# Kernel tuning notes

Measured on AMD Instinct MI355X. Metric: run time of the kernel, lower is better.

Reference implementation:

```python
import jax, jax.numpy as jnp
import numpy as np

N = 50000   # nodes
E = 200000  # edges (avg degree ~4, pose-graph-like sparsity)
F_IN = 512
NEG_SLOPE = 0.01  # F.leaky_relu default


def _softmax_aggr(src_feat, dst, num_nodes):
    # torch_geometric SoftmaxAggregation(t=1): per-destination, per-feature
    # alpha = softmax(x_j), out = sum_j alpha * x_j
    m = jax.ops.segment_max(src_feat, dst, num_segments=num_nodes)  # [N,F]
    m = jnp.where(jnp.isfinite(m), m, 0.0)  # empty segments -> -inf guard
    e = jnp.exp(src_feat - m[dst])                                   # [E,F]
    denom = jax.ops.segment_sum(e, dst, num_segments=num_nodes)      # [N,F]
    num = jax.ops.segment_sum(e * src_feat, dst, num_segments=num_nodes)
    return num / jnp.maximum(denom, 1e-16)  # 0 for isolated nodes


def setup_inputs() -> dict:
    key = jax.random.key(0)
    ks = jax.random.split(key, 9)
    inp = {
        "x": jax.random.normal(ks[0], (N, F_IN), dtype=jnp.float32),
        "W1_rel": jax.random.normal(ks[1], (513, 256), dtype=jnp.float32) * 0.04,
        "b1_rel": jnp.zeros((256,), dtype=jnp.float32),
        "W1_root": jax.random.normal(ks[2], (513, 256), dtype=jnp.float32) * 0.04,
        "W2_rel": jax.random.normal(ks[3], (257, 64), dtype=jnp.float32) * 0.06,
        "b2_rel": jnp.zeros((64,), dtype=jnp.float32),
        "W2_root": jax.random.normal(ks[4], (257, 64), dtype=jnp.float32) * 0.06,
        "Wp": jax.random.normal(ks[5], (65, 3), dtype=jnp.float32) * 0.1,
        "bp": jnp.zeros((3,), dtype=jnp.float32),
        "Wr": jax.random.normal(ks[6], (65, 4), dtype=jnp.float32) * 0.1,
        "br": jnp.zeros((4,), dtype=jnp.float32),
        "edge_index": jax.random.randint(ks[7], (2, E), 0, N, dtype=jnp.int64),
    }
    return inp


def reference(x, W1_rel, b1_rel, W1_root, W2_rel, b2_rel, W2_root,
              Wp, bp, Wr, br, edge_index):
    src, dst = edge_index[0], edge_index[1]
    node_index = jnp.arange(x.shape[0], dtype=x.dtype)[:, None]  # [N,1]

    # dropout is identity in eval mode
    h = jnp.concatenate([x, node_index], axis=1)  # [N,513]

    # GraphConv(513,256, aggr='softmax'): lin_rel(softmax_aggr(x_j)) + lin_root(x)
    agg1 = _softmax_aggr(h[src], dst, x.shape[0])               # [N,513]
    h = agg1 @ W1_rel + b1_rel + h @ W1_root                     # [N,256]
    h = jnp.where(h >= 0, h, NEG_SLOPE * h)

    h = jnp.concatenate([h, node_index], axis=1)  # [N,257]

    # GraphConv(257,64) default aggr='add'
    agg2 = jax.ops.segment_sum(h[src], dst, num_segments=x.shape[0])  # [N,257]
    h = agg2 @ W2_rel + b2_rel + h @ W2_root                           # [N,64]
    h = jnp.where(h >= 0, h, NEG_SLOPE * h)

    h = jnp.concatenate([h, node_index], axis=1)  # [N,65]

    position = h @ Wp + bp                         # [N,3]
    rotation = h @ Wr + br                         # [N,4]
    norm = jnp.linalg.norm(rotation, axis=1, keepdims=True)
    rotation = rotation / jnp.maximum(norm, 1e-12)  # F.normalize

    return jnp.concatenate([position, rotation], axis=1)  # [N,7]
```

## Files before the change

### kernel.cpp

```cpp
#include <hip/hip_runtime.h>

#define NNODES 50000
#define NEDGES 200000
#define NSCANB ((NNODES + 255) / 256)

typedef short  bf16x8 __attribute__((ext_vector_type(8)));
typedef float  f32x4  __attribute__((ext_vector_type(4)));
typedef unsigned int u32x4 __attribute__((ext_vector_type(4)));

__device__ __forceinline__ unsigned short f2bf(float f) {
    union { float f; unsigned int u; } c; c.f = f;
    unsigned int r = c.u + 0x7fffu + ((c.u >> 16) & 1u);
    return (unsigned short)(r >> 16);
}
__device__ __forceinline__ float bf2f(unsigned short h) {
    union { unsigned int u; float f; } c; c.u = ((unsigned int)h) << 16;
    return c.f;
}
__device__ __forceinline__ float bflo(unsigned int v) {
    union { unsigned int u; float f; } c; c.u = v << 16;
    return c.f;
}
__device__ __forceinline__ float bfhi(unsigned int v) {
    union { unsigned int u; float f; } c; c.u = v & 0xffff0000u;
    return c.f;
}

#define PREP_B1 (256 * 1024)
#define PREP_B2 (64 * 512)
#define PREP_XC (NNODES * 64)
__global__ __launch_bounds__(256) void k_prepcount(const float* __restrict__ x,
                                                   const float* __restrict__ W1_rel,
                                                   const float* __restrict__ W1_root,
                                                   const float* __restrict__ W2_rel,
                                                   const float* __restrict__ W2_root,
                                                   const int* __restrict__ ei,
                                                   int* __restrict__ deg,
                                                   unsigned short* __restrict__ Bt1,
                                                   unsigned short* __restrict__ Bt2,
                                                   unsigned short* __restrict__ xb) {
    const int gtid = blockIdx.x * 256 + threadIdx.x;
    const int GS = gridDim.x * 256;
    for (int e = gtid; e < NEDGES; e += GS) atomicAdd(&deg[ei[NEDGES + e]], 1);
    for (int i = gtid; i < PREP_B1; i += GS) {
        int n = i >> 10, k = i & 1023;
        float v = (k < 512) ? W1_rel[k * 256 + n] : W1_root[(k - 512) * 256 + n];
        Bt1[i] = f2bf(v);
    }
    for (int i = gtid; i < PREP_B2; i += GS) {
        int n = i >> 9, k = i & 511;
        float v = (k < 256) ? W2_rel[k * 64 + n] : W2_root[(k - 256) * 64 + n];
        Bt2[i] = f2bf(v);
    }
    for (int i = gtid; i < PREP_XC; i += GS) {
        int n = i >> 6, c8 = (i & 63) * 8;
        const float* xp = x + (size_t)n * 512 + c8;
        float4 a = *(const float4*)xp;
        float4 bb = *(const float4*)(xp + 4);
        unsigned short o[8];
        o[0] = f2bf(a.x); o[1] = f2bf(a.y); o[2] = f2bf(a.z); o[3] = f2bf(a.w);
        o[4] = f2bf(bb.x); o[5] = f2bf(bb.y); o[6] = f2bf(bb.z); o[7] = f2bf(bb.w);
        *(u32x4*)(xb + (size_t)n * 512 + c8) = *(const u32x4*)o;
    }
}

__global__ __launch_bounds__(256) void k_scanA(const int* __restrict__ deg,
                                               int* __restrict__ rs,
                                               int* __restrict__ partials) {
    __shared__ int sm[256];
    int t = threadIdx.x, i = blockIdx.x * 256 + t;
    int v = (i < NNODES) ? deg[i] : 0;
    sm[t] = v;
    __syncthreads();
#pragma unroll
    for (int off = 1; off < 256; off <<= 1) {
        int u = (t >= off) ? sm[t - off] : 0;
        __syncthreads();
        sm[t] += u;
        __syncthreads();
    }
    if (i < NNODES) rs[i] = sm[t] - v;
    if (t == 255) partials[blockIdx.x] = sm[255];
}

__global__ __launch_bounds__(256) void k_scanC2(int* __restrict__ rs,
                                                const int* __restrict__ partials,
                                                int* __restrict__ cursor) {
    __shared__ int sm[256];
    int t = threadIdx.x, b = blockIdx.x;
    sm[t] = (t < b && t < NSCANB) ? partials[t] : 0;
    __syncthreads();
#pragma unroll
    for (int off = 128; off; off >>= 1) {
        if (t < off) sm[t] += sm[t + off];
        __syncthreads();
    }
    int off0 = sm[0];
    int i = b * 256 + t;
    if (i < NNODES) {
        int rv = rs[i] + off0;
        rs[i] = rv;
        cursor[i] = rv;
    }
    if (i == 0) rs[NNODES] = NEDGES;
}

__global__ void k_scatter(const int* __restrict__ ei, int* __restrict__ cursor,
                          int* __restrict__ srcs) {
    int e = blockIdx.x * 256 + threadIdx.x;
    if (e < NEDGES) {
        int d = ei[NEDGES + e];
        int p = atomicAdd(&cursor[d], 1);
        srcs[p] = ei[e];
    }
}

__global__ __launch_bounds__(256) void k_agg1(const unsigned short* __restrict__ xb,
                                              const int* __restrict__ rs,
                                              const int* __restrict__ srcs,
                                              unsigned short* __restrict__ AggBuf) {
    int wv = threadIdx.x >> 6;
    int lane = threadIdx.x & 63;
    int n = blockIdx.x * 4 + wv;
    int e0 = rs[n], e1 = rs[n + 1];
    float nu[8], de[8];
#pragma unroll
    for (int j = 0; j < 8; ++j) { nu[j] = 0.f; de[j] = 0.f; }
    int e = e0;
    for (; e + 1 < e1; e += 2) {
        int s0 = srcs[e], s1 = srcs[e + 1];
        u32x4 r0 = *(const u32x4*)(xb + (size_t)s0 * 512 + lane * 8);
        u32x4 r1 = *(const u32x4*)(xb + (size_t)s1 * 512 + lane * 8);
#pragma unroll
        for (int p = 0; p < 4; ++p) {
            float v0 = bflo(r0[p]), v1 = bfhi(r0[p]);
            float E0 = __expf(v0), E1 = __expf(v1);
            de[2 * p] += E0; nu[2 * p] += E0 * v0;
            de[2 * p + 1] += E1; nu[2 * p + 1] += E1 * v1;
        }
#pragma unroll
        for (int p = 0; p < 4; ++p) {
            float v0 = bflo(r1[p]), v1 = bfhi(r1[p]);
            float E0 = __expf(v0), E1 = __expf(v1);
            de[2 * p] += E0; nu[2 * p] += E0 * v0;
            de[2 * p + 1] += E1; nu[2 * p + 1] += E1 * v1;
        }
    }
    if (e < e1) {
        int s0 = srcs[e];
        u32x4 r0 = *(const u32x4*)(xb + (size_t)s0 * 512 + lane * 8);
#pragma unroll
        for (int p = 0; p < 4; ++p) {
            float v0 = bflo(r0[p]), v1 = bfhi(r0[p]);
            float E0 = __expf(v0), E1 = __expf(v1);
            de[2 * p] += E0; nu[2 * p] += E0 * v0;
            de[2 * p + 1] += E1; nu[2 * p + 1] += E1 * v1;
        }
    }
    unsigned short o[8];
#pragma unroll
    for (int j = 0; j < 8; ++j) o[j] = f2bf(nu[j] / fmaxf(de[j], 1e-16f));
    *(u32x4*)(AggBuf + (size_t)n * 512 + lane * 8) = *(const u32x4*)o;
}

__global__ __launch_bounds__(256) void k_agg2(const int* __restrict__ rs,
                                              const int* __restrict__ srcs,
                                              const unsigned short* __restrict__ H1,
                                              unsigned short* __restrict__ Seg) {
    int wv = threadIdx.x >> 6;
    int lane = threadIdx.x & 63;
    int n = blockIdx.x * 4 + wv;
    int e0 = rs[n], e1 = rs[n + 1];
    float a[4] = {0.f, 0.f, 0.f, 0.f};
    int e = e0;
    for (; e + 1 < e1; e += 2) {
        int s0 = srcs[e], s1 = srcs[e + 1];
        uint2 r0 = *(const uint2*)(H1 + (size_t)s0 * 256 + lane * 4);
        uint2 r1 = *(const uint2*)(H1 + (size_t)s1 * 256 + lane * 4);
        a[0] += bflo(r0.x) + bflo(r1.x);
        a[1] += bfhi(r0.x) + bfhi(r1.x);
        a[2] += bflo(r0.y) + bflo(r1.y);
        a[3] += bfhi(r0.y) + bfhi(r1.y);
    }
    if (e < e1) {
        uint2 r0 = *(const uint2*)(H1 + (size_t)srcs[e] * 256 + lane * 4);
        a[0] += bflo(r0.x); a[1] += bfhi(r0.x);
        a[2] += bflo(r0.y); a[3] += bfhi(r0.y);
    }
    uint2 o;
    o.x = (unsigned int)f2bf(a[0]) | ((unsigned int)f2bf(a[1]) << 16);
    o.y = (unsigned int)f2bf(a[2]) | ((unsigned int)f2bf(a[3]) << 16);
    *(uint2*)(Seg + (size_t)n * 256 + lane * 4) = o;
}

__global__ __launch_bounds__(256, 5) void k_gemm1(const unsigned short* __restrict__ A1,
                                                  const unsigned short* __restrict__ A2,
                                                  const unsigned short* __restrict__ Bt,
                                                  const int* __restrict__ rs,
                                                  const int* __restrict__ srcs,
                                                  const float* __restrict__ r1,
                                                  const float* __restrict__ r2,
                                                  const float* __restrict__ bias,
                                                  unsigned short* __restrict__ outp) {
    constexpr int BM = 64, BN = 128, BK = 64;
    __shared__ __align__(16) unsigned short As[2][BM * BK];
    __shared__ __align__(16) unsigned short Bs[2][BN * BK];
    __shared__ float s1t[BM];

    const int tid = threadIdx.x;
    const int w = tid >> 6;
    const int lane = tid & 63;
    const int lm = lane & 15;
    const int quad = lane >> 4;
    const int wr = w >> 1;
    const int wc = w & 1;
    const int rowbase = blockIdx.y * BM;
    const int colbase = blockIdx.x * BN;
    const int wrow = wr * 32;
    const int wcol = wc * 64;

    const int rsub = lane >> 3;
    const int csw = (lane & 7) ^ rsub;

    f32x4 acc[2][4];
#pragma unroll
    for (int mi = 0; mi < 2; ++mi)
#pragma unroll
        for (int ni = 0; ni < 4; ++ni) acc[mi][ni] = (f32x4){0.f, 0.f, 0.f, 0.f};

    auto stage = [&](unsigned short* Asb, unsigned short* Bsb, int kt) {
        const unsigned short* Ab = (kt < 512) ? A1 : A2;
        int kof = (kt < 512) ? kt : kt - 512;
#pragma unroll
        for (int l = 0; l < 2; ++l) {
            int r = w * 16 + l * 8;
            int gr = rowbase + r + rsub;
            if (gr >= NNODES) gr = NNODES - 1;
            const unsigned short* gp = Ab + (size_t)gr * 512 + kof + csw * 8;
            __builtin_amdgcn_global_load_lds(
                (const __attribute__((address_space(1))) void*)gp,
                (__attribute__((address_space(3))) void*)(Asb + r * BK), 16, 0, 0);
        }
#pragma unroll
        for (int l = 0; l < 4; ++l) {
            int r = w * 32 + l * 8;
            const unsigned short* gp = Bt + (size_t)(colbase + r + rsub) * 1024 + kt + csw * 8;
            __builtin_amdgcn_global_load_lds(
                (const __attribute__((address_space(1))) void*)gp,
                (__attribute__((address_space(3))) void*)(Bsb + r * BK), 16, 0, 0);
        }
    };

    auto compute = [&](const unsigned short* Asb, const unsigned short* Bsb) {
#pragma unroll
        for (int kk = 0; kk < BK; kk += 32) {
            const int kidx = (kk >> 3) + quad;
            const int phys = kidx ^ (lm & 7);
            bf16x8 af[2], bfr[4];
#pragma unroll
            for (int mi = 0; mi < 2; ++mi)
                af[mi] = __builtin_bit_cast(bf16x8,
                    *(const u32x4*)(Asb + (wrow + mi * 16 + lm) * BK + phys * 8));
#pragma unroll
            for (int ni = 0; ni < 4; ++ni)
                bfr[ni] = __builtin_bit_cast(bf16x8,
                    *(const u32x4*)(Bsb + (wcol + ni * 16 + lm) * BK + phys * 8));
#pragma unroll
            for (int mi = 0; mi < 2; ++mi)
#pragma unroll
                for (int ni = 0; ni < 4; ++ni)
                    acc[mi][ni] = __builtin_amdgcn_mfma_f32_16x16x32_bf16(
                        af[mi], bfr[ni], acc[mi][ni], 0, 0, 0);
        }
    };

    stage(As[0], Bs[0], 0);
#pragma unroll 1
    for (int t = 0; t < 16; t += 2) {
        stage(As[1], Bs[1], (t + 1) * BK);
        asm volatile("s_waitcnt vmcnt(6)" ::: "memory");
        __builtin_amdgcn_s_barrier();
        __builtin_amdgcn_sched_barrier(0);
        compute(As[0], Bs[0]);
        __builtin_amdgcn_s_barrier();
        if (t + 2 < 16) {
            stage(As[0], Bs[0], (t + 2) * BK);
            asm volatile("s_waitcnt vmcnt(6)" ::: "memory");
        } else {
            asm volatile("s_waitcnt vmcnt(0)" ::: "memory");
        }
        __builtin_amdgcn_s_barrier();
        __builtin_amdgcn_sched_barrier(0);
        compute(As[1], Bs[1]);
        __builtin_amdgcn_s_barrier();
    }

    if (tid < BM) {
        int grow = rowbase + tid;
        float r_ = 0.f;
        if (grow < NNODES) {
            int e0 = rs[grow], e1 = rs[grow + 1];
            float m = -INFINITY, d = 0.f, q = 0.f;
            for (int e = e0; e < e1; ++e) {
                float v = (float)srcs[e];
                float nm = fmaxf(m, v);
                float sc = __expf(m - nm), ee = __expf(v - nm);
                d = d * sc + ee;
                q = q * sc + ee * v;
                m = nm;
            }
            r_ = q / fmaxf(d, 1e-16f);
        }
        s1t[tid] = r_;
    }
    __syncthreads();

#pragma unroll
    for (int ni = 0; ni < 4; ++ni) {
        int gc = colbase + wcol + ni * 16 + lm;
        float r1v = r1[gc], r2v = r2[gc], bv = bias[gc];
#pragma unroll
        for (int mi = 0; mi < 2; ++mi) {
#pragma unroll
            for (int r = 0; r < 4; ++r) {
                int lrow = wrow + mi * 16 + quad * 4 + r;
                int grow = rowbase + lrow;
                if (grow < NNODES) {
                    float v = acc[mi][ni][r] + s1t[lrow] * r1v + (float)grow * r2v + bv;
                    v = (v >= 0.f) ? v : 0.01f * v;
                    outp[(size_t)grow * 256 + gc] = f2bf(v);
                }
            }
        }
    }
}

__global__ __launch_bounds__(256) void k_gemm2h(const unsigned short* __restrict__ A1,
                                                const unsigned short* __restrict__ A2,
                                                const unsigned short* __restrict__ Bt,
                                                const int* __restrict__ rs,
                                                const int* __restrict__ srcs,
                                                const float* __restrict__ r1,
                                                const float* __restrict__ r2,
                                                const float* __restrict__ bias,
                                                const float* __restrict__ Wp,
                                                const float* __restrict__ bp,
                                                const float* __restrict__ Wr,
                                                const float* __restrict__ br,
                                                float* __restrict__ out) {
    constexpr int BM = 64, BN = 64, BK = 64;
    __shared__ __align__(16) unsigned short As[2][BM * BK];
    __shared__ __align__(16) unsigned short Bs[2][BN * BK];
    __shared__ float h2t[BM * 65];
    __shared__ float s1t[BM];

    const int tid = threadIdx.x;
    const int w = tid >> 6;
    const int lane = tid & 63;
    const int lm = lane & 15;
    const int quad = lane >> 4;
    const int rowbase = blockIdx.x * BM;
    const int wrow = w * 16;

    const int rsub = lane >> 3;
    const int csw = (lane & 7) ^ rsub;

    f32x4 acc[4];
#pragma unroll
    for (int ni = 0; ni < 4; ++ni) acc[ni] = (f32x4){0.f, 0.f, 0.f, 0.f};

    auto stage = [&](unsigned short* Asb, unsigned short* Bsb, int kt) {
        const unsigned short* Ab = (kt < 256) ? A1 : A2;
        int kof = (kt < 256) ? kt : kt - 256;
#pragma unroll
        for (int l = 0; l < 2; ++l) {
            int r = w * 16 + l * 8;
            int gr = rowbase + r + rsub;
            if (gr >= NNODES) gr = NNODES - 1;
            const unsigned short* gp = Ab + (size_t)gr * 256 + kof + csw * 8;
            __builtin_amdgcn_global_load_lds(
                (const __attribute__((address_space(1))) void*)gp,
                (__attribute__((address_space(3))) void*)(Asb + r * BK), 16, 0, 0);
        }
#pragma unroll
        for (int l = 0; l < 2; ++l) {
            int r = w * 16 + l * 8;
            const unsigned short* gp = Bt + (size_t)(r + rsub) * 512 + kt + csw * 8;
            __builtin_amdgcn_global_load_lds(
                (const __attribute__((address_space(1))) void*)gp,
                (__attribute__((address_space(3))) void*)(Bsb + r * BK), 16, 0, 0);
        }
    };

    auto compute = [&](const unsigned short* Asb, const unsigned short* Bsb) {
#pragma unroll
        for (int kk = 0; kk < BK; kk += 32) {
            const int kidx = (kk >> 3) + quad;
            const int phys = kidx ^ (lm & 7);
            bf16x8 af;
            af = __builtin_bit_cast(bf16x8,
                *(const u32x4*)(Asb + (wrow + lm) * BK + phys * 8));
            bf16x8 bfr[4];
#pragma unroll
            for (int ni = 0; ni < 4; ++ni)
                bfr[ni] = __builtin_bit_cast(bf16x8,
                    *(const u32x4*)(Bsb + (ni * 16 + lm) * BK + phys * 8));
#pragma unroll
            for (int ni = 0; ni < 4; ++ni)
                acc[ni] = __builtin_amdgcn_mfma_f32_16x16x32_bf16(
                    af, bfr[ni], acc[ni], 0, 0, 0);
        }
    };

    stage(As[0], Bs[0], 0);
#pragma unroll 1
    for (int t = 0; t < 8; t += 2) {
        stage(As[1], Bs[1], (t + 1) * BK);
        asm volatile("s_waitcnt vmcnt(4)" ::: "memory");
        __builtin_amdgcn_s_barrier();
        __builtin_amdgcn_sched_barrier(0);
        compute(As[0], Bs[0]);
        __builtin_amdgcn_s_barrier();
        if (t + 2 < 8) {
            stage(As[0], Bs[0], (t + 2) * BK);
            asm volatile("s_waitcnt vmcnt(4)" ::: "memory");
        } else {
            asm volatile("s_waitcnt vmcnt(0)" ::: "memory");
        }
        __builtin_amdgcn_s_barrier();
        __builtin_amdgcn_sched_barrier(0);
        compute(As[1], Bs[1]);
        __builtin_amdgcn_s_barrier();
    }

    if (tid < BM) {
        int grow = rowbase + tid;
        float si = 0.f;
        if (grow < NNODES) {
            int e0 = rs[grow], e1 = rs[grow + 1];
            for (int e = e0; e < e1; ++e) si += (float)srcs[e];
        }
        s1t[tid] = si;
    }
    __syncthreads();

#pragma unroll
    for (int ni = 0; ni < 4; ++ni) {
        int gc = ni * 16 + lm;
        float r1v = r1[gc], r2v = r2[gc], bv = bias[gc];
#pragma unroll
        for (int r = 0; r < 4; ++r) {
            int lrow = wrow + quad * 4 + r;
            int grow = rowbase + lrow;
            float v = acc[ni][r] + s1t[lrow] * r1v + (float)grow * r2v + bv;
            v = (v >= 0.f) ? v : 0.01f * v;
            h2t[lrow * 65 + gc] = v;
        }
    }
    __syncthreads();

    if (tid < BM) {
        int grow = rowbase + tid;
        if (grow < NNODES) {
            const float* hv = h2t + tid * 65;
            float idx = (float)grow;
            float p0 = 0.f, p1 = 0.f, p2 = 0.f;
            float r0 = 0.f, r1a = 0.f, r2a = 0.f, r3 = 0.f;
#pragma unroll 8
            for (int c = 0; c < 64; ++c) {
                float v = hv[c];
                p0 += v * Wp[c * 3 + 0];
                p1 += v * Wp[c * 3 + 1];
                p2 += v * Wp[c * 3 + 2];
                r0 += v * Wr[c * 4 + 0];
                r1a += v * Wr[c * 4 + 1];
                r2a += v * Wr[c * 4 + 2];
                r3 += v * Wr[c * 4 + 3];
            }
            p0 += idx * Wp[64 * 3 + 0] + bp[0];
            p1 += idx * Wp[64 * 3 + 1] + bp[1];
            p2 += idx * Wp[64 * 3 + 2] + bp[2];
            r0 += idx * Wr[64 * 4 + 0] + br[0];
            r1a += idx * Wr[64 * 4 + 1] + br[1];
            r2a += idx * Wr[64 * 4 + 2] + br[2];
            r3 += idx * Wr[64 * 4 + 3] + br[3];
            float nrm = fmaxf(sqrtf(r0 * r0 + r1a * r1a + r2a * r2a + r3 * r3), 1e-12f);
            float* op = out + (size_t)grow * 7;
            op[0] = p0; op[1] = p1; op[2] = p2;
            op[3] = r0 / nrm; op[4] = r1a / nrm; op[5] = r2a / nrm; op[6] = r3 / nrm;
        }
    }
}

extern "C" void kernel_launch(void* const* d_in, const int* in_sizes, int n_in,
                              void* d_out, int out_size, void* d_ws, size_t ws_size,
                              hipStream_t stream) {
    const float* x       = (const float*)d_in[0];
    const float* W1_rel  = (const float*)d_in[1];
    const float* b1      = (const float*)d_in[2];
    const float* W1_root = (const float*)d_in[3];
    const float* W2_rel  = (const float*)d_in[4];
    const float* b2      = (const float*)d_in[5];
    const float* W2_root = (const float*)d_in[6];
    const float* Wp      = (const float*)d_in[7];
    const float* bp      = (const float*)d_in[8];
    const float* Wr      = (const float*)d_in[9];
    const float* br      = (const float*)d_in[10];
    const int*   ei      = (const int*)d_in[11];
    float* out = (float*)d_out;

    char* ws = (char*)d_ws;
    size_t off = 0;
    auto alloc = [&](size_t bytes) {
        size_t o = off;
        off = (off + bytes + 255) & ~(size_t)255;
        return (void*)(ws + o);
    };
    int*   deg       = (int*)alloc(NNODES * 4);
    int*   cursor    = (int*)alloc(NNODES * 4);
    int*   row_start = (int*)alloc((NNODES + 1) * 4);
    int*   srcs      = (int*)alloc(NEDGES * 4);
    int*   partials  = (int*)alloc(NSCANB * 4);
    unsigned short* xb     = (unsigned short*)alloc((size_t)NNODES * 512 * 2);
    unsigned short* AggBuf = (unsigned short*)alloc((size_t)NNODES * 512 * 2);
    unsigned short* H1     = (unsigned short*)alloc((size_t)NNODES * 256 * 2);
    unsigned short* Seg    = (unsigned short*)alloc((size_t)NNODES * 256 * 2);
    unsigned short* Bt1    = (unsigned short*)alloc(256 * 1024 * 2);
    unsigned short* Bt2    = (unsigned short*)alloc(64 * 512 * 2);

    hipMemsetAsync(deg, 0, NNODES * 4, stream);

    k_prepcount<<<2048, 256, 0, stream>>>(
        x, W1_rel, W1_root, W2_rel, W2_root, ei, deg, Bt1, Bt2, xb);

    k_scanA<<<NSCANB, 256, 0, stream>>>(deg, row_start, partials);
    k_scanC2<<<NSCANB, 256, 0, stream>>>(row_start, partials, cursor);
    k_scatter<<<(NEDGES + 255) / 256, 256, 0, stream>>>(ei, cursor, srcs);

    k_agg1<<<NNODES / 4, 256, 0, stream>>>(xb, row_start, srcs, AggBuf);

    k_gemm1<<<dim3(2, (NNODES + 63) / 64), 256, 0, stream>>>(
        AggBuf, xb, Bt1, row_start, srcs, W1_rel + 512 * 256, W1_root + 512 * 256, b1, H1);

    k_agg2<<<NNODES / 4, 256, 0, stream>>>(row_start, srcs, H1, Seg);

    k_gemm2h<<<(NNODES + 63) / 64, 256, 0, stream>>>(
        Seg, H1, Bt2, row_start, srcs, W2_rel + 256 * 64, W2_root + 256 * 64, b2,
        Wp, bp, Wr, br, out);
}
```

Measured before the change: 353.7 us.

## Unroll gather loops by four and simplify gemm2h to single-buffered staging

The edge-gather loops in both aggregation kernels are unrolled to four edges per iteration, so more independent row loads are in flight per wave. The occupancy hint is removed from the first GEMM's launch bounds. The second GEMM replaces its hand-scheduled double-buffered LDS pipeline with a single buffer and plain barriers, which frees LDS and may raise occupancy. In exchange it loses the overlap between loading and computing.

```diff
diff --git a/kernel.cpp b/kernel.cpp
--- a/kernel.cpp
+++ b/kernel.cpp
@@ -12,10 +12,6 @@
     union { float f; unsigned int u; } c; c.f = f;
     unsigned int r = c.u + 0x7fffu + ((c.u >> 16) & 1u);
     return (unsigned short)(r >> 16);
-}
-__device__ __forceinline__ float bf2f(unsigned short h) {
-    union { unsigned int u; float f; } c; c.u = ((unsigned int)h) << 16;
-    return c.f;
 }
 __device__ __forceinline__ float bflo(unsigned int v) {
     union { unsigned int u; float f; } c; c.u = v << 16;
@@ -126,36 +122,36 @@
     float nu[8], de[8];
 #pragma unroll
     for (int j = 0; j < 8; ++j) { nu[j] = 0.f; de[j] = 0.f; }
+
+    auto accum = [&](u32x4 r) {
+#pragma unroll
+        for (int p = 0; p < 4; ++p) {
+            float v0 = bflo(r[p]), v1 = bfhi(r[p]);
+            float E0 = __expf(v0), E1 = __expf(v1);
+            de[2 * p] += E0; nu[2 * p] += E0 * v0;
+            de[2 * p + 1] += E1; nu[2 * p + 1] += E1 * v1;
+        }
+    };
+
     int e = e0;
-    for (; e + 1 < e1; e += 2) {
+    for (; e + 3 < e1; e += 4) {
+        int s0 = srcs[e], s1 = srcs[e + 1], s2 = srcs[e + 2], s3 = srcs[e + 3];
+        u32x4 r0 = *(const u32x4*)(xb + (size_t)s0 * 512 + lane * 8);
+        u32x4 r1 = *(const u32x4*)(xb + (size_t)s1 * 512 + lane * 8);
+        u32x4 r2 = *(const u32x4*)(xb + (size_t)s2 * 512 + lane * 8);
+        u32x4 r3 = *(const u32x4*)(xb + (size_t)s3 * 512 + lane * 8);
+        accum(r0); accum(r1); accum(r2); accum(r3);
+    }
+    if (e + 1 < e1) {
         int s0 = srcs[e], s1 = srcs[e + 1];
         u32x4 r0 = *(const u32x4*)(xb + (size_t)s0 * 512 + lane * 8);
         u32x4 r1 = *(const u32x4*)(xb + (size_t)s1 * 512 + lane * 8);
-#pragma unroll
-        for (int p = 0; p < 4; ++p) {
-            float v0 = bflo(r0[p]), v1 = bfhi(r0[p]);
-            float E0 = __expf(v0), E1 = __expf(v1);
-            de[2 * p] += E0; nu[2 * p] += E0 * v0;
-            de[2 * p + 1] += E1; nu[2 * p + 1] += E1 * v1;
-        }
-#pragma unroll
-        for (int p = 0; p < 4; ++p) {
-            float v0 = bflo(r1[p]), v1 = bfhi(r1[p]);
-            float E0 = __expf(v0), E1 = __expf(v1);
-            de[2 * p] += E0; nu[2 * p] += E0 * v0;
-            de[2 * p + 1] += E1; nu[2 * p + 1] += E1 * v1;
-        }
+        accum(r0); accum(r1);
+        e += 2;
     }
     if (e < e1) {
-        int s0 = srcs[e];
-        u32x4 r0 = *(const u32x4*)(xb + (size_t)s0 * 512 + lane * 8);
-#pragma unroll
-        for (int p = 0; p < 4; ++p) {
-            float v0 = bflo(r0[p]), v1 = bfhi(r0[p]);
-            float E0 = __expf(v0), E1 = __expf(v1);
-            de[2 * p] += E0; nu[2 * p] += E0 * v0;
-            de[2 * p + 1] += E1; nu[2 * p + 1] += E1 * v1;
-        }
+        u32x4 r0 = *(const u32x4*)(xb + (size_t)srcs[e] * 512 + lane * 8);
+        accum(r0);
     }
     unsigned short o[8];
 #pragma unroll
@@ -172,20 +168,31 @@
     int n = blockIdx.x * 4 + wv;
     int e0 = rs[n], e1 = rs[n + 1];
     float a[4] = {0.f, 0.f, 0.f, 0.f};
+
+    auto accum = [&](uint2 r) {
+        a[0] += bflo(r.x); a[1] += bfhi(r.x);
+        a[2] += bflo(r.y); a[3] += bfhi(r.y);
+    };
+
     int e = e0;
-    for (; e + 1 < e1; e += 2) {
+    for (; e + 3 < e1; e += 4) {
+        int s0 = srcs[e], s1 = srcs[e + 1], s2 = srcs[e + 2], s3 = srcs[e + 3];
+        uint2 r0 = *(const uint2*)(H1 + (size_t)s0 * 256 + lane * 4);
+        uint2 r1 = *(const uint2*)(H1 + (size_t)s1 * 256 + lane * 4);
+        uint2 r2 = *(const uint2*)(H1 + (size_t)s2 * 256 + lane * 4);
+        uint2 r3 = *(const uint2*)(H1 + (size_t)s3 * 256 + lane * 4);
+        accum(r0); accum(r1); accum(r2); accum(r3);
+    }
+    if (e + 1 < e1) {
         int s0 = srcs[e], s1 = srcs[e + 1];
         uint2 r0 = *(const uint2*)(H1 + (size_t)s0 * 256 + lane * 4);
         uint2 r1 = *(const uint2*)(H1 + (size_t)s1 * 256 + lane * 4);
-        a[0] += bflo(r0.x) + bflo(r1.x);
-        a[1] += bfhi(r0.x) + bfhi(r1.x);
-        a[2] += bflo(r0.y) + bflo(r1.y);
-        a[3] += bfhi(r0.y) + bfhi(r1.y);
+        accum(r0); accum(r1);
+        e += 2;
     }
     if (e < e1) {
         uint2 r0 = *(const uint2*)(H1 + (size_t)srcs[e] * 256 + lane * 4);
-        a[0] += bflo(r0.x); a[1] += bfhi(r0.x);
-        a[2] += bflo(r0.y); a[3] += bfhi(r0.y);
+        accum(r0);
     }
     uint2 o;
     o.x = (unsigned int)f2bf(a[0]) | ((unsigned int)f2bf(a[1]) << 16);
@@ -193,15 +200,15 @@
     *(uint2*)(Seg + (size_t)n * 256 + lane * 4) = o;
 }
 
-__global__ __launch_bounds__(256, 5) void k_gemm1(const unsigned short* __restrict__ A1,
-                                                  const unsigned short* __restrict__ A2,
-                                                  const unsigned short* __restrict__ Bt,
-                                                  const int* __restrict__ rs,
-                                                  const int* __restrict__ srcs,
-                                                  const float* __restrict__ r1,
-                                                  const float* __restrict__ r2,
-                                                  const float* __restrict__ bias,
-                                                  unsigned short* __restrict__ outp) {
+__global__ __launch_bounds__(256) void k_gemm1(const unsigned short* __restrict__ A1,
+                                               const unsigned short* __restrict__ A2,
+                                               const unsigned short* __restrict__ Bt,
+                                               const int* __restrict__ rs,
+                                               const int* __restrict__ srcs,
+                                               const float* __restrict__ r1,
+                                               const float* __restrict__ r2,
+                                               const float* __restrict__ bias,
+                                               unsigned short* __restrict__ outp) {
     constexpr int BM = 64, BN = 128, BK = 64;
     __shared__ __align__(16) unsigned short As[2][BM * BK];
     __shared__ __align__(16) unsigned short Bs[2][BN * BK];
@@ -349,8 +356,8 @@
                                                 const float* __restrict__ br,
                                                 float* __restrict__ out) {
     constexpr int BM = 64, BN = 64, BK = 64;
-    __shared__ __align__(16) unsigned short As[2][BM * BK];
-    __shared__ __align__(16) unsigned short Bs[2][BN * BK];
+    __shared__ __align__(16) unsigned short As[BM * BK];
+    __shared__ __align__(16) unsigned short Bs[BN * BK];
     __shared__ float h2t[BM * 65];
     __shared__ float s1t[BM];
 
@@ -369,7 +376,7 @@
 #pragma unroll
     for (int ni = 0; ni < 4; ++ni) acc[ni] = (f32x4){0.f, 0.f, 0.f, 0.f};
 
-    auto stage = [&](unsigned short* Asb, unsigned short* Bsb, int kt) {
+    for (int kt = 0; kt < 512; kt += BK) {
         const unsigned short* Ab = (kt < 256) ? A1 : A2;
         int kof = (kt < 256) ? kt : kt - 256;
 #pragma unroll
@@ -380,7 +387,7 @@
             const unsigned short* gp = Ab + (size_t)gr * 256 + kof + csw * 8;
             __builtin_amdgcn_global_load_lds(
                 (const __attribute__((address_space(1))) void*)gp,
-                (__attribute__((address_space(3))) void*)(Asb + r * BK), 16, 0, 0);
+                (__attribute__((address_space(3))) void*)(As + r * BK), 16, 0, 0);
         }
 #pragma unroll
         for (int l = 0; l < 2; ++l) {
@@ -388,49 +395,27 @@
             const unsigned short* gp = Bt + (size_t)(r + rsub) * 512 + kt + csw * 8;
             __builtin_amdgcn_global_load_lds(
                 (const __attribute__((address_space(1))) void*)gp,
-                (__attribute__((address_space(3))) void*)(Bsb + r * BK), 16, 0, 0);
-        }
-    };
-
-    auto compute = [&](const unsigned short* Asb, const unsigned short* Bsb) {
+                (__attribute__((address_space(3))) void*)(Bs + r * BK), 16, 0, 0);
+        }
+        __syncthreads();
 #pragma unroll
         for (int kk = 0; kk < BK; kk += 32) {
             const int kidx = (kk >> 3) + quad;
             const int phys = kidx ^ (lm & 7);
             bf16x8 af;
             af = __builtin_bit_cast(bf16x8,
-                *(const u32x4*)(Asb + (wrow + lm) * BK + phys * 8));
+                *(const u32x4*)(As + (wrow + lm) * BK + phys * 8));
             bf16x8 bfr[4];
 #pragma unroll
             for (int ni = 0; ni < 4; ++ni)
                 bfr[ni] = __builtin_bit_cast(bf16x8,
-                    *(const u32x4*)(Bsb + (ni * 16 + lm) * BK + phys * 8));
+                    *(const u32x4*)(Bs + (ni * 16 + lm) * BK + phys * 8));
 #pragma unroll
             for (int ni = 0; ni < 4; ++ni)
                 acc[ni] = __builtin_amdgcn_mfma_f32_16x16x32_bf16(
                     af, bfr[ni], acc[ni], 0, 0, 0);
         }
-    };
-
-    stage(As[0], Bs[0], 0);
-#pragma unroll 1
-    for (int t = 0; t < 8; t += 2) {
-        stage(As[1], Bs[1], (t + 1) * BK);
-        asm volatile("s_waitcnt vmcnt(4)" ::: "memory");
-        __builtin_amdgcn_s_barrier();
-        __builtin_amdgcn_sched_barrier(0);
-        compute(As[0], Bs[0]);
-        __builtin_amdgcn_s_barrier();
-        if (t + 2 < 8) {
-            stage(As[0], Bs[0], (t + 2) * BK);
-            asm volatile("s_waitcnt vmcnt(4)" ::: "memory");
-        } else {
-            asm volatile("s_waitcnt vmcnt(0)" ::: "memory");
-        }
-        __builtin_amdgcn_s_barrier();
-        __builtin_amdgcn_sched_barrier(0);
-        compute(As[1], Bs[1]);
-        __builtin_amdgcn_s_barrier();
+        __syncthreads();
     }
 
     if (tid < BM) {
```

After: 339.7 us. 1.04x faster.
